# Kernel tuning notes

Measured on AMD Instinct MI355X. Metric: run time of the kernel, lower is better.

## Reference

```python
import jax, jax.numpy as jnp
import numpy as np

IN_FEATURES = 4096
OUT_FEATURES = max(IN_FEATURES - 2, 1)
BATCH = 4096


def setup_inputs() -> dict:
    key = jax.random.key(0)
    k1, k2, k3 = jax.random.split(key, 3)
    stdv = 1.0 / np.sqrt(IN_FEATURES)
    x = jax.random.normal(k1, (BATCH, IN_FEATURES), dtype=jnp.float32)
    weight = jax.random.uniform(k2, (OUT_FEATURES, IN_FEATURES), dtype=jnp.float32,
                                minval=-stdv, maxval=stdv)
    bias = jax.random.uniform(k3, (OUT_FEATURES,), dtype=jnp.float32,
                              minval=-stdv, maxval=stdv)
    return {"input": x, "weight": weight, "bias": bias}


def reference(input, weight, bias):
    # Faithful to source: i, j = (0, 3) are never updated in the loop, so every
    # column n accumulates into output[:, 0:3]:
    #   output[:, 0:3] += input[:, n:n+1] @ weight[0:3, n:n+1].T + bias[0:3]
    # Summed over all n, this is a skinny GEMM plus bias added N times.
    B, N = input.shape
    M = weight.shape[0]
    w = min(3, M)  # slice width (python int, static)
    # (B, w) accumulated contribution
    contrib = input @ weight[:w].T + jnp.asarray(N, input.dtype) * bias[:w]
    out = jnp.zeros((B, M), dtype=input.dtype).at[:, :w].set(contrib)
    return out
```

## Files before the change

### kernel.cpp

```cpp
#include <hip/hip_runtime.h>

#define IN_F   4096
#define OUT_F  4094
#define BATCH_ 4096
#define WCOLS  3

__global__ __launch_bounds__(256) void zero_fill_kernel(float4* __restrict__ out,
                                                        long n4) {
    long i = (long)blockIdx.x * blockDim.x + threadIdx.x;
    long stride = (long)gridDim.x * blockDim.x;
    const float4 z = make_float4(0.f, 0.f, 0.f, 0.f);
    for (; i < n4; i += stride) {
        out[i] = z;
    }
}

__global__ __launch_bounds__(256) void skinny_dot_kernel(const float* __restrict__ in,
                                                         const float* __restrict__ w,
                                                         const float* __restrict__ bias,
                                                         float* __restrict__ out) {
    const int b   = blockIdx.x;
    const int tid = threadIdx.x;

    const float4* __restrict__ row = (const float4*)(in + (long)b * IN_F);
    const float4* __restrict__ w0  = (const float4*)(w);
    const float4* __restrict__ w1  = (const float4*)(w + IN_F);
    const float4* __restrict__ w2  = (const float4*)(w + 2 * IN_F);

    float s0 = 0.f, s1 = 0.f, s2 = 0.f;

    #pragma unroll 4
    for (int i = tid; i < IN_F / 4; i += 256) {
        float4 x = row[i];
        float4 a = w0[i];
        float4 c = w1[i];
        float4 d = w2[i];
        s0 = fmaf(x.x, a.x, fmaf(x.y, a.y, fmaf(x.z, a.z, fmaf(x.w, a.w, s0))));
        s1 = fmaf(x.x, c.x, fmaf(x.y, c.y, fmaf(x.z, c.z, fmaf(x.w, c.w, s1))));
        s2 = fmaf(x.x, d.x, fmaf(x.y, d.y, fmaf(x.z, d.z, fmaf(x.w, d.w, s2))));
    }

    #pragma unroll
    for (int off = 32; off > 0; off >>= 1) {
        s0 += __shfl_down(s0, off);
        s1 += __shfl_down(s1, off);
        s2 += __shfl_down(s2, off);
    }

    __shared__ float red[4][WCOLS];
    const int wave = tid >> 6;
    const int lane = tid & 63;
    if (lane == 0) {
        red[wave][0] = s0;
        red[wave][1] = s1;
        red[wave][2] = s2;
    }
    __syncthreads();

    if (tid < WCOLS) {
        float t = red[0][tid] + red[1][tid] + red[2][tid] + red[3][tid];
        out[(long)b * OUT_F + tid] = t + (float)IN_F * bias[tid];
    }
}

extern "C" void kernel_launch(void* const* d_in, const int* in_sizes, int n_in,
                              void* d_out, int out_size, void* d_ws, size_t ws_size,
                              hipStream_t stream) {
    const float* in   = (const float*)d_in[0];
    const float* w    = (const float*)d_in[1];
    const float* bias = (const float*)d_in[2];
    float* out = (float*)d_out;

    const long n4 = (long)BATCH_ * OUT_F / 4;
    zero_fill_kernel<<<2048, 256, 0, stream>>>((float4*)out, n4);

    skinny_dot_kernel<<<BATCH_, 256, 0, stream>>>(in, w, bias, out);
}
```

Baseline: 28.51 us.

## Fuse output zero-fill into per-row dot kernel with nontemporal memory ops

Removes the separate zero-fill kernel: each block now zeroes its own output row with 8-byte nontemporal stores, alongside its 3-column dot product. The input row is read with a nontemporal load hint, while the reused weight rows stay on normal loads. This drops one kernel launch and the serialization between the fill and compute phases, so the read and write streams can overlap. In exchange, stores narrow from 16-byte to 8-byte vectors, because the row stride of 4094 floats only guarantees 8-byte alignment, and the write pattern is now tied to per-row block scheduling.

New measurement: 35.91 us. 1.26x slower.

```diff
diff --git a/kernel.cpp b/kernel.cpp
--- a/kernel.cpp
+++ b/kernel.cpp
@@ -5,39 +5,39 @@
 #define BATCH_ 4096
 #define WCOLS  3
 
-__global__ __launch_bounds__(256) void zero_fill_kernel(float4* __restrict__ out,
-                                                        long n4) {
-    long i = (long)blockIdx.x * blockDim.x + threadIdx.x;
-    long stride = (long)gridDim.x * blockDim.x;
-    const float4 z = make_float4(0.f, 0.f, 0.f, 0.f);
-    for (; i < n4; i += stride) {
-        out[i] = z;
-    }
-}
+typedef float f32x4 __attribute__((ext_vector_type(4)));
+typedef float f32x2 __attribute__((ext_vector_type(2)));
 
-__global__ __launch_bounds__(256) void skinny_dot_kernel(const float* __restrict__ in,
-                                                         const float* __restrict__ w,
-                                                         const float* __restrict__ bias,
-                                                         float* __restrict__ out) {
+__global__ __launch_bounds__(256) void fused_row_kernel(const float* __restrict__ in,
+                                                        const float* __restrict__ w,
+                                                        const float* __restrict__ bias,
+                                                        float* __restrict__ out) {
     const int b   = blockIdx.x;
     const int tid = threadIdx.x;
 
-    const float4* __restrict__ row = (const float4*)(in + (long)b * IN_F);
-    const float4* __restrict__ w0  = (const float4*)(w);
-    const float4* __restrict__ w1  = (const float4*)(w + IN_F);
-    const float4* __restrict__ w2  = (const float4*)(w + 2 * IN_F);
+    const f32x4* __restrict__ row = (const f32x4*)(in + (long)b * IN_F);
+    const f32x4* __restrict__ w0  = (const f32x4*)(w);
+    const f32x4* __restrict__ w1  = (const f32x4*)(w + IN_F);
+    const f32x4* __restrict__ w2  = (const f32x4*)(w + 2 * IN_F);
 
     float s0 = 0.f, s1 = 0.f, s2 = 0.f;
 
     #pragma unroll 4
     for (int i = tid; i < IN_F / 4; i += 256) {
-        float4 x = row[i];
-        float4 a = w0[i];
-        float4 c = w1[i];
-        float4 d = w2[i];
+        f32x4 x = __builtin_nontemporal_load(&row[i]);
+        f32x4 a = w0[i];
+        f32x4 c = w1[i];
+        f32x4 d = w2[i];
         s0 = fmaf(x.x, a.x, fmaf(x.y, a.y, fmaf(x.z, a.z, fmaf(x.w, a.w, s0))));
         s1 = fmaf(x.x, c.x, fmaf(x.y, c.y, fmaf(x.z, c.z, fmaf(x.w, c.w, s1))));
         s2 = fmaf(x.x, d.x, fmaf(x.y, d.y, fmaf(x.z, d.z, fmaf(x.w, d.w, s2))));
+    }
+
+    f32x2* __restrict__ orow = (f32x2*)(out + (long)b * OUT_F);
+    const f32x2 z2 = {0.f, 0.f};
+    #pragma unroll
+    for (int i = tid; i < OUT_F / 2; i += 256) {
+        __builtin_nontemporal_store(z2, &orow[i]);
     }
 
     #pragma unroll
@@ -71,8 +71,5 @@
     const float* bias = (const float*)d_in[2];
     float* out = (float*)d_out;
 
-    const long n4 = (long)BATCH_ * OUT_F / 4;
-    zero_fill_kernel<<<2048, 256, 0, stream>>>((float4*)out, n4);
-
-    skinny_dot_kernel<<<BATCH_, 256, 0, stream>>>(in, w, bias, out);
+    fused_row_kernel<<<BATCH_, 256, 0, stream>>>(in, w, bias, out);
 }
```
